# Performance work log

Measured on AMD Instinct MI355X. Metric: run time of the kernel, lower is better.

## Reference

```python
import jax, jax.numpy as jnp
import numpy as np

SR = 16000
N_FFT = 512
HOP = 160
WIN = 320
N_MELS = 80
FMIN = 0.0
FMAX = 8000.0
PAD_TO = 8
BLANK = 27.0
PREEMPH = 0.97
LOG_EPS = 2.0 ** -24
STD_EPS = 1e-5


def _hz_to_mel(f):
    # Slaney mel scale (librosa default, htk=False)
    f = np.asarray(f, dtype=np.float64)
    f_sp = 200.0 / 3.0
    mels = f / f_sp
    min_log_hz = 1000.0
    min_log_mel = min_log_hz / f_sp
    logstep = np.log(6.4) / 27.0
    return np.where(f >= min_log_hz,
                    min_log_mel + np.log(np.maximum(f, 1e-10) / min_log_hz) / logstep,
                    mels)


def _mel_to_hz(m):
    m = np.asarray(m, dtype=np.float64)
    f_sp = 200.0 / 3.0
    freqs = m * f_sp
    min_log_hz = 1000.0
    min_log_mel = min_log_hz / f_sp
    logstep = np.log(6.4) / 27.0
    return np.where(m >= min_log_mel,
                    min_log_hz * np.exp(logstep * (m - min_log_mel)),
                    freqs)


def mel_filterbank():
    # librosa.filters.mel(16000, 512, n_mels=80, fmin=0, fmax=8000), slaney norm
    fftfreqs = np.linspace(0.0, SR / 2.0, 1 + N_FFT // 2)
    mel_f = _mel_to_hz(np.linspace(_hz_to_mel(FMIN), _hz_to_mel(FMAX), N_MELS + 2))
    fdiff = np.diff(mel_f)
    ramps = mel_f[:, None] - fftfreqs[None, :]
    lower = -ramps[:-2] / fdiff[:-1, None]
    upper = ramps[2:] / fdiff[1:, None]
    weights = np.maximum(0.0, np.minimum(lower, upper))
    enorm = 2.0 / (mel_f[2:N_MELS + 2] - mel_f[:N_MELS])  # slaney norm
    weights *= enorm[:, None]
    return weights.astype(np.float32)  # [80, 257]


def _window():
    # periodic hann of length 320, zero-padded to 512 (centered), as in nnAudio STFT
    n = np.arange(WIN)
    w = 0.5 - 0.5 * np.cos(2.0 * np.pi * n / WIN)
    pad = (N_FFT - WIN) // 2
    return np.pad(w, (pad, pad)).astype(np.float32)  # [512]


def setup_inputs() -> dict:
    key = jax.random.key(0)
    k1, k2 = jax.random.split(key)
    B, L = 32, 240000
    x = 0.1 * jax.random.normal(k1, (B, L), dtype=jnp.float32)
    xn = jax.random.randint(k2, (B,), 160000, L + 1, dtype=jnp.int64)
    filterbank = jnp.asarray(mel_filterbank())
    return {"x": x, "xn": xn, "filterbank": filterbank}


def reference(x, xn, filterbank):
    B, L = x.shape
    seq_len = (xn // HOP + 1).astype(jnp.int64)  # floor((L+pad-512)/160)+1, pad=512

    # pre-emphasis (eval mode: dither=0)
    y = jnp.concatenate([x[:, :1], x[:, 1:] - PREEMPH * x[:, :-1]], axis=1)

    # center=True reflect pad by n_fft//2
    y = jnp.pad(y, ((0, 0), (N_FFT // 2, N_FFT // 2)), mode="reflect")

    # frame: T = L//HOP + 1
    T = L // HOP + 1
    idx = jnp.arange(T)[:, None] * HOP + jnp.arange(N_FFT)[None, :]  # [T, 512]
    frames = y[:, idx]  # [B, T, 512]
    win = jnp.asarray(_window())
    spec = jnp.fft.rfft(frames * win, axis=-1)  # [B, T, 257] complex
    power = jnp.real(spec) ** 2 + jnp.imag(spec) ** 2  # |X|^2 (sqrt then ^2 in torch)

    mel = jnp.einsum("mf,btf->bmt", filterbank, power)  # [B, 80, T]
    logmel = jnp.log(mel + LOG_EPS)

    # ragged per-sample, per-feature mean/std (std unbiased, ddof=1) over valid frames
    valid = (jnp.arange(T)[None, :] < seq_len[:, None]).astype(logmel.dtype)  # [B, T]
    n = seq_len.astype(logmel.dtype)[:, None]  # [B, 1]
    vm = valid[:, None, :]  # [B, 1, T]
    mean = jnp.sum(logmel * vm, axis=-1) / n  # [B, 80]
    centered = (logmel - mean[..., None]) * vm
    var = jnp.sum(centered * centered, axis=-1) / (n - 1.0)
    std = jnp.sqrt(var) + STD_EPS
    out = (logmel - mean[..., None]) / std[..., None]

    # zero out invalid frames, then pad T to multiple of PAD_TO with BLANK
    out = out * vm
    pad_amt = T % PAD_TO
    if pad_amt != 0:
        out = jnp.pad(out, ((0, 0), (0, 0), (0, PAD_TO - pad_amt)),
                      constant_values=BLANK)
    return out, seq_len
```

## Files before the change

### kernel.cpp

```cpp
#include <hip/hip_runtime.h>
#include <math.h>

constexpr int BATCH = 32;
constexpr int LEN   = 240000;
constexpr int HOPS  = 160;
constexpr int T     = 1501;
constexpr int TOUT  = 1504;
constexpr int NMEL  = 80;
constexpr int NBIN  = 257;
constexpr int PAIRS = 751;
constexpr int CMAX  = 20;
constexpr int WSTR  = 25;
constexpr int P1OFF = 520;
constexpr float PRE     = 0.97f;
constexpr float LOG_EPS = 5.9604644775390625e-08f;
constexpr float STD_EPS = 1e-5f;
constexpr float BLANK_V = 27.0f;

constexpr size_t LOGMEL_ELTS = (size_t)BATCH * T * NMEL;

struct cpx { float r, i; };
__device__ __forceinline__ cpx cmul(cpx a, cpx b){ return {a.r*b.r - a.i*b.i, a.r*b.i + a.i*b.r}; }
__device__ __forceinline__ cpx cadd(cpx a, cpx b){ return {a.r+b.r, a.i+b.i}; }
__device__ __forceinline__ cpx csub(cpx a, cpx b){ return {a.r-b.r, a.i-b.i}; }

__device__ __forceinline__ void dft8(cpx* a) {
  const float s = 0.70710678118654752f;
  cpx b0 = cadd(a[0],a[4]), b1 = cadd(a[1],a[5]), b2 = cadd(a[2],a[6]), b3 = cadd(a[3],a[7]);
  cpx t0 = csub(a[0],a[4]), t1 = csub(a[1],a[5]), t2 = csub(a[2],a[6]), t3 = csub(a[3],a[7]);
  cpx e0 = t0;
  cpx e1 = { s*(t1.r + t1.i), s*(t1.i - t1.r) };
  cpx e2 = { t2.i, -t2.r };
  cpx e3 = { s*(t3.i - t3.r), -s*(t3.r + t3.i) };
  cpx c0 = cadd(b0,b2), c1 = cadd(b1,b3), c2 = csub(b0,b2), c3 = csub(b1,b3);
  cpx f0 = cadd(e0,e2), f1 = cadd(e1,e3), f2 = csub(e0,e2), f3 = csub(e1,e3);
  a[0] = cadd(c0,c1); a[4] = csub(c0,c1);
  a[2] = { c2.r + c3.i, c2.i - c3.r }; a[6] = { c2.r - c3.i, c2.i + c3.r };
  a[1] = cadd(f0,f1); a[5] = csub(f0,f1);
  a[3] = { f2.r + f3.i, f2.i - f3.r }; a[7] = { f2.r - f3.i, f2.i + f3.r };
}

__device__ __forceinline__ int read_n(const int* xn32, int b) {
  int probe = xn32[1];
  int v = (probe == 0) ? xn32[2 * b] : xn32[b];
  return v / HOPS + 1;
}

__global__ __launch_bounds__(64) void k_prep(const float* __restrict__ fb,
                                             int* __restrict__ lc,
                                             float* __restrict__ wg,
                                             float* __restrict__ ps) {
  const int m = blockIdx.x;
  const int l = threadIdx.x;
  ps[m * 64 + l] = 0.f;
  int first = 1 << 20, last = -1;
  for (int it = 0; it < 5; ++it) {
    int f = it * 64 + l;
    float w = (f < NBIN) ? fb[m * NBIN + f] : 0.f;
    unsigned long long mk = __ballot(w != 0.f);
    if (mk) {
      int lo = __ffsll(mk) - 1;
      int hi = 63 - __clzll(mk);
      if (first > NBIN) first = it * 64 + lo;
      last = it * 64 + hi;
    }
  }
  int cnt = (last >= first) ? last - first + 1 : 0;
  if (cnt > CMAX) cnt = CMAX;
  if (first > NBIN) first = 0;
  if (l == 0) lc[m] = first | (cnt << 16);
  if (l < CMAX) wg[m * CMAX + l] = (l < cnt) ? fb[m * NBIN + first + l] : 0.f;
}

__global__ __launch_bounds__(256) void k_logmel(const float* __restrict__ x,
    const int* __restrict__ lc, const float* __restrict__ wg,
    const int* __restrict__ xn32,
    float* __restrict__ logmel, float* __restrict__ ps) {
  __shared__ float shw[512];
  __shared__ float swg[NMEL * WSTR];
  __shared__ int   slc[NMEL];
  __shared__ float W[4][1024];
  __shared__ float vbuf[4][160];
  __shared__ int   sbw[4];

  const int tid = threadIdx.x;
  const int wid = tid >> 6;
  const int l   = tid & 63;

  for (int i = tid; i < 512; i += 256) {
    float w = 0.f;
    if (i >= 96 && i < 416)
      w = 0.5f - 0.5f * __cosf((float)(i - 96) * (6.283185307179586f / 320.f));
    shw[i] = w;
  }
  for (int i = tid; i < NMEL * CMAX; i += 256)
    swg[(i / CMAX) * WSTR + (i % CMAX)] = wg[i];
  if (tid < NMEL) slc[tid] = lc[tid];
  __syncthreads();

  float* Tre = W[wid];
  float* Tim = Tre + 512;

  const int pair = blockIdx.x * 4 + wid;
  const int b  = pair / PAIRS;
  const int q  = pair % PAIRS;
  const int t0 = 2 * q;
  const float* xb = x + (size_t)b * LEN;
  const int nb = read_n(xn32, b);

  cpx a[8];
  const int s0x = t0 * HOPS - 161;
  const bool interior = (s0x >= 0) && (s0x + 480 < LEN);
  if (interior) {
    for (int i = l; i < 481; i += 64) Tre[i] = xb[s0x + i];
    __builtin_amdgcn_wave_barrier();
    #pragma unroll
    for (int j = 0; j < 8; ++j) {
      int n = l + 64 * j;
      cpx z = {0.f, 0.f};
      if (n >= 96 && n < 416) {
        float w = shw[n];
        z.r = w * (Tre[n - 95] - PRE * Tre[n - 96]);
        z.i = w * (Tre[n + 65] - PRE * Tre[n + 64]);
      }
      a[j] = z;
    }
    __builtin_amdgcn_wave_barrier();
  } else {
    #pragma unroll
    for (int j = 0; j < 8; ++j) {
      int n = l + 64 * j;
      cpx z = {0.f, 0.f};
      if (n >= 96 && n < 416) {
        float w = shw[n];
        int p0 = t0 * HOPS + n - 256;
        int p1 = p0 + HOPS;
        int q0 = p0 < 0 ? -p0 : (p0 >= LEN ? 2 * LEN - 2 - p0 : p0);
        int q1 = p1 < 0 ? -p1 : (p1 >= LEN ? 2 * LEN - 2 - p1 : p1);
        float y0 = (q0 == 0) ? xb[0] : (xb[q0] - PRE * xb[q0 - 1]);
        float y1 = (q1 == 0) ? xb[0] : (xb[q1] - PRE * xb[q1 - 1]);
        z.r = w * y0; z.i = w * y1;
      }
      a[j] = z;
    }
  }

  dft8(a);
  {
    float sv, cv; __sincosf(-6.283185307179586f * (float)l / 512.f, &sv, &cv);
    cpx w1 = {cv, sv}, cur = w1;
    #pragma unroll
    for (int p = 1; p < 8; ++p) { a[p] = cmul(a[p], cur); cur = cmul(cur, w1); }
  }
  #pragma unroll
  for (int p = 0; p < 8; ++p) { int idx = 64 * p + (l ^ (8 * p)); Tre[idx] = a[p].r; Tim[idx] = a[p].i; }
  __builtin_amdgcn_wave_barrier();

  const int ph = l >> 3, lo8 = l & 7;
  #pragma unroll
  for (int m2 = 0; m2 < 8; ++m2) {
    int idx = 64 * ph + ((lo8 + 8 * m2) ^ (8 * ph));
    a[m2] = {Tre[idx], Tim[idx]};
  }
  dft8(a);
  {
    float sv, cv; __sincosf(-6.283185307179586f * (float)lo8 / 64.f, &sv, &cv);
    cpx w1 = {cv, sv}, cur = w1;
    #pragma unroll
    for (int r = 1; r < 8; ++r) { a[r] = cmul(a[r], cur); cur = cmul(cur, w1); }
  }
  __builtin_amdgcn_wave_barrier();
  #pragma unroll
  for (int r = 0; r < 8; ++r) { int idx = 64 * ph + 8 * (r ^ ph) + (lo8 ^ ph); Tre[idx] = a[r].r; Tim[idx] = a[r].i; }
  __builtin_amdgcn_wave_barrier();
  #pragma unroll
  for (int m1 = 0; m1 < 8; ++m1) {
    int idx = 64 * ph + 8 * (lo8 ^ ph) + (m1 ^ ph);
    a[m1] = {Tre[idx], Tim[idx]};
  }
  dft8(a);
  __builtin_amdgcn_wave_barrier();
  #pragma unroll
  for (int s = 0; s < 8; ++s) { int k = ph + 8 * lo8 + 64 * s; Tre[k] = a[s].r; Tim[k] = a[s].i; }
  __builtin_amdgcn_wave_barrier();

  float P0[4], P1[4];
  #pragma unroll
  for (int c = 0; c < 4; ++c) {
    int k  = l + 64 * c;
    int km = (512 - k) & 511;
    float zr = Tre[k], zi = Tim[k], mr = Tre[km], mi = Tim[km];
    float f0r = 0.5f * (zr + mr), f0i = 0.5f * (zi - mi);
    float f1r = 0.5f * (zi + mi), f1i = 0.5f * (mr - zr);
    P0[c] = f0r * f0r + f0i * f0i;
    P1[c] = f1r * f1r + f1i * f1i;
  }
  float pN0 = 0.f, pN1 = 0.f;
  if (l == 0) { float zr = Tre[256], zi = Tim[256]; pN0 = zr * zr; pN1 = zi * zi; }
  __builtin_amdgcn_wave_barrier();
  #pragma unroll
  for (int c = 0; c < 4; ++c) { int k = l + 64 * c; Tre[k] = P0[c]; Tre[P1OFF + k] = P1[c]; }
  if (l == 0) { Tre[256] = pN0; Tre[P1OFF + 256] = pN1; }
  __builtin_amdgcn_wave_barrier();

  auto melrow = [&](int f, int m) -> float {
    int meta = slc[m];
    int lo = meta & 0xffff;
    const float* pw = &swg[m * WSTR];
    const float* pp = &Tre[(f ? P1OFF : 0) + lo];
    float acc = 0.f;
    #pragma unroll
    for (int j = 0; j < CMAX; ++j) acc += pp[j] * pw[j];
    return __logf(acc + LOG_EPS);
  };

  size_t base0 = ((size_t)b * T + t0) * NMEL;
  {
    float lv = melrow(0, l);
    logmel[base0 + l] = lv;
    vbuf[wid][l] = (t0 < nb) ? lv : 0.f;
  }
  {
    bool ok = (t0 + 1) < T;
    float lv = ok ? melrow(1, l) : 0.f;
    if (ok) logmel[base0 + NMEL + l] = lv;
    vbuf[wid][80 + l] = (ok && (t0 + 1) < nb) ? lv : 0.f;
  }
  if (l < 32) {
    int f = l >> 4, m = 64 + (l & 15);
    bool ok = (t0 + f) < T;
    float lv = ok ? melrow(f, m) : 0.f;
    if (ok) logmel[base0 + (size_t)f * NMEL + m] = lv;
    vbuf[wid][f * 80 + m] = (ok && (t0 + f) < nb) ? lv : 0.f;
  }
  if (l == 0) sbw[wid] = b;
  __syncthreads();

  if (tid < NMEL) {
    const int b0 = (blockIdx.x * 4) / PAIRS;
    const bool strad = ((blockIdx.x * 4 + 3) / PAIRS) != b0;
    float s0 = 0.f, q0 = 0.f, s1 = 0.f, q1 = 0.f;
    #pragma unroll
    for (int w = 0; w < 4; ++w) {
      float v0 = vbuf[w][tid], v1 = vbuf[w][80 + tid];
      if (sbw[w] == b0) { s0 += v0 + v1; q0 += v0 * v0 + v1 * v1; }
      else              { s1 += v0 + v1; q1 += v0 * v0 + v1 * v1; }
    }
    atomicAdd(&ps[b0 * 160 + tid], s0);
    atomicAdd(&ps[b0 * 160 + 80 + tid], q0);
    if (strad) {
      atomicAdd(&ps[(b0 + 1) * 160 + tid], s1);
      atomicAdd(&ps[(b0 + 1) * 160 + 80 + tid], q1);
    }
  }
}

__global__ __launch_bounds__(256) void k_apply(const float* __restrict__ logmel,
    const float* __restrict__ ps, const int* __restrict__ xn32,
    float* __restrict__ out, float* __restrict__ outseq) {
  const int bid = blockIdx.x;
  const int b = bid / 47, c = bid % 47;
  const int tbase = c * 32;
  __shared__ float tile[32 * 81];
  __shared__ float smean[80], sistd[80];
  const int tid = threadIdx.x;
  const int n = read_n(xn32, b);
  if (tid < 80) {
    float S = ps[b * 160 + tid], S2 = ps[b * 160 + 80 + tid];
    float fn = (float)n;
    float mean = S / fn;
    float var = (S2 - fn * mean * mean) / (fn - 1.f);
    var = var < 0.f ? 0.f : var;
    smean[tid] = mean;
    sistd[tid] = 1.f / (sqrtf(var) + STD_EPS);
  }
  __syncthreads();

  for (int e = tid; e < 640; e += 256) {
    int tt = e / 20, v = e % 20;
    int t = tbase + tt;
    int m0 = 4 * v;
    float4 val;
    if (t >= T)      val = make_float4(BLANK_V, BLANK_V, BLANK_V, BLANK_V);
    else if (t >= n) val = make_float4(0.f, 0.f, 0.f, 0.f);
    else {
      const float4 g = *(const float4*)&logmel[((size_t)b * T + t) * NMEL + m0];
      val.x = (g.x - smean[m0])     * sistd[m0];
      val.y = (g.y - smean[m0 + 1]) * sistd[m0 + 1];
      val.z = (g.z - smean[m0 + 2]) * sistd[m0 + 2];
      val.w = (g.w - smean[m0 + 3]) * sistd[m0 + 3];
    }
    float* tp = &tile[tt * 81 + m0];
    tp[0] = val.x; tp[1] = val.y; tp[2] = val.z; tp[3] = val.w;
  }
  __syncthreads();
  for (int e = tid; e < 640; e += 256) {
    int m = e >> 3, v = e & 7;
    int tt0 = 4 * v;
    float4 o;
    o.x = tile[(tt0    ) * 81 + m];
    o.y = tile[(tt0 + 1) * 81 + m];
    o.z = tile[(tt0 + 2) * 81 + m];
    o.w = tile[(tt0 + 3) * 81 + m];
    *(float4*)&out[((size_t)b * NMEL + m) * TOUT + tbase + tt0] = o;
  }
  if (c == 0 && tid == 0) outseq[b] = (float)n;
}

extern "C" void kernel_launch(void* const* d_in, const int* in_sizes, int n_in,
                              void* d_out, int out_size, void* d_ws, size_t ws_size,
                              hipStream_t stream) {
  const float* x  = (const float*)d_in[0];
  const int*   xn = (const int*)d_in[1];
  const float* fb = (const float*)d_in[2];

  float* out    = (float*)d_out;
  float* outseq = out + (size_t)BATCH * NMEL * TOUT;

  float* logmel = (float*)d_ws;
  int*   lc = (int*)(logmel + LOGMEL_ELTS);
  float* wg = (float*)(lc + NMEL);
  float* ps = wg + NMEL * CMAX;

  k_prep  <<<NMEL, 64, 0, stream>>>(fb, lc, wg, ps);
  k_logmel<<<(BATCH * PAIRS) / 4, 256, 0, stream>>>(x, lc, wg, xn, logmel, ps);
  k_apply <<<BATCH * 47, 256, 0, stream>>>(logmel, ps, xn, out, outseq);
}
```

Before: 131.3 us.

## Interleave complex data as float2 in LDS and pack mel pair compute

Stores FFT scratch as interleaved float2 (real, imag) instead of split real and imag planes, so each LDS access moves a complex pair. The power spectra of the two frames are packed into float2 so one mel dot-product loop serves both frames. The Hann window is now computed inline rather than held in a shared table, and the k_logmel launch bounds request 6 blocks per SM. k_apply tiles 64 frames per block instead of 32, which halves the block count and needs a bounds guard on the tail tile.

```diff
diff --git a/kernel.cpp b/kernel.cpp
--- a/kernel.cpp
+++ b/kernel.cpp
@@ -10,8 +10,7 @@
 constexpr int NBIN  = 257;
 constexpr int PAIRS = 751;
 constexpr int CMAX  = 20;
-constexpr int WSTR  = 25;
-constexpr int P1OFF = 520;
+constexpr int WSTR  = 21;
 constexpr float PRE     = 0.97f;
 constexpr float LOG_EPS = 5.9604644775390625e-08f;
 constexpr float STD_EPS = 1e-5f;
@@ -19,25 +18,35 @@
 
 constexpr size_t LOGMEL_ELTS = (size_t)BATCH * T * NMEL;
 
-struct cpx { float r, i; };
-__device__ __forceinline__ cpx cmul(cpx a, cpx b){ return {a.r*b.r - a.i*b.i, a.r*b.i + a.i*b.r}; }
-__device__ __forceinline__ cpx cadd(cpx a, cpx b){ return {a.r+b.r, a.i+b.i}; }
-__device__ __forceinline__ cpx csub(cpx a, cpx b){ return {a.r-b.r, a.i-b.i}; }
-
-__device__ __forceinline__ void dft8(cpx* a) {
+typedef __attribute__((ext_vector_type(2))) float v2f;
+
+__device__ __forceinline__ v2f cmul(v2f a, v2f b) {
+  v2f r;
+  r.x = a.x * b.x - a.y * b.y;
+  r.y = a.x * b.y + a.y * b.x;
+  return r;
+}
+
+__device__ __forceinline__ void dft8(v2f* a) {
   const float s = 0.70710678118654752f;
-  cpx b0 = cadd(a[0],a[4]), b1 = cadd(a[1],a[5]), b2 = cadd(a[2],a[6]), b3 = cadd(a[3],a[7]);
-  cpx t0 = csub(a[0],a[4]), t1 = csub(a[1],a[5]), t2 = csub(a[2],a[6]), t3 = csub(a[3],a[7]);
-  cpx e0 = t0;
-  cpx e1 = { s*(t1.r + t1.i), s*(t1.i - t1.r) };
-  cpx e2 = { t2.i, -t2.r };
-  cpx e3 = { s*(t3.i - t3.r), -s*(t3.r + t3.i) };
-  cpx c0 = cadd(b0,b2), c1 = cadd(b1,b3), c2 = csub(b0,b2), c3 = csub(b1,b3);
-  cpx f0 = cadd(e0,e2), f1 = cadd(e1,e3), f2 = csub(e0,e2), f3 = csub(e1,e3);
-  a[0] = cadd(c0,c1); a[4] = csub(c0,c1);
-  a[2] = { c2.r + c3.i, c2.i - c3.r }; a[6] = { c2.r - c3.i, c2.i + c3.r };
-  a[1] = cadd(f0,f1); a[5] = csub(f0,f1);
-  a[3] = { f2.r + f3.i, f2.i - f3.r }; a[7] = { f2.r - f3.i, f2.i + f3.r };
+  v2f b0 = a[0] + a[4], b1 = a[1] + a[5], b2 = a[2] + a[6], b3 = a[3] + a[7];
+  v2f t0 = a[0] - a[4], t1 = a[1] - a[5], t2 = a[2] - a[6], t3 = a[3] - a[7];
+  v2f e0 = t0, e1, e2, e3;
+  e1.x = s * (t1.x + t1.y); e1.y = s * (t1.y - t1.x);
+  e2.x = t2.y;              e2.y = -t2.x;
+  e3.x = s * (t3.y - t3.x); e3.y = -s * (t3.x + t3.y);
+  v2f c0 = b0 + b2, c1 = b1 + b3, c2 = b0 - b2, c3 = b1 - b3;
+  v2f f0 = e0 + e2, f1 = e1 + e3, f2 = e0 - e2, f3 = e1 - e3;
+  a[0] = c0 + c1; a[4] = c0 - c1;
+  a[2].x = c2.x + c3.y; a[2].y = c2.y - c3.x;
+  a[6].x = c2.x - c3.y; a[6].y = c2.y + c3.x;
+  a[1] = f0 + f1; a[5] = f0 - f1;
+  a[3].x = f2.x + f3.y; a[3].y = f2.y - f3.x;
+  a[7].x = f2.x - f3.y; a[7].y = f2.y + f3.x;
+}
+
+__device__ __forceinline__ float hann(int n) {
+  return 0.5f - 0.5f * __cosf((float)(n - 96) * (6.283185307179586f / 320.f));
 }
 
 __device__ __forceinline__ int read_n(const int* xn32, int b) {
@@ -72,34 +81,26 @@
   if (l < CMAX) wg[m * CMAX + l] = (l < cnt) ? fb[m * NBIN + first + l] : 0.f;
 }
 
-__global__ __launch_bounds__(256) void k_logmel(const float* __restrict__ x,
+__global__ __launch_bounds__(256, 6) void k_logmel(const float* __restrict__ x,
     const int* __restrict__ lc, const float* __restrict__ wg,
     const int* __restrict__ xn32,
     float* __restrict__ logmel, float* __restrict__ ps) {
-  __shared__ float shw[512];
+  __shared__ v2f   Wv[4][512];
   __shared__ float swg[NMEL * WSTR];
   __shared__ int   slc[NMEL];
-  __shared__ float W[4][1024];
-  __shared__ float vbuf[4][160];
+  __shared__ v2f   vbuf[4][NMEL];
   __shared__ int   sbw[4];
 
   const int tid = threadIdx.x;
   const int wid = tid >> 6;
   const int l   = tid & 63;
 
-  for (int i = tid; i < 512; i += 256) {
-    float w = 0.f;
-    if (i >= 96 && i < 416)
-      w = 0.5f - 0.5f * __cosf((float)(i - 96) * (6.283185307179586f / 320.f));
-    shw[i] = w;
-  }
   for (int i = tid; i < NMEL * CMAX; i += 256)
     swg[(i / CMAX) * WSTR + (i % CMAX)] = wg[i];
   if (tid < NMEL) slc[tid] = lc[tid];
   __syncthreads();
 
-  float* Tre = W[wid];
-  float* Tim = Tre + 512;
+  v2f* Wvw = Wv[wid];
 
   const int pair = blockIdx.x * 4 + wid;
   const int b  = pair / PAIRS;
@@ -108,20 +109,23 @@
   const float* xb = x + (size_t)b * LEN;
   const int nb = read_n(xn32, b);
 
-  cpx a[8];
+  v2f a[8];
   const int s0x = t0 * HOPS - 161;
   const bool interior = (s0x >= 0) && (s0x + 480 < LEN);
   if (interior) {
-    for (int i = l; i < 481; i += 64) Tre[i] = xb[s0x + i];
+    float* Ts = (float*)Wvw;
+    for (int i = l; i < 481; i += 64) Ts[i] = xb[s0x + i];
     __builtin_amdgcn_wave_barrier();
     #pragma unroll
     for (int j = 0; j < 8; ++j) {
       int n = l + 64 * j;
-      cpx z = {0.f, 0.f};
+      v2f z = {0.f, 0.f};
       if (n >= 96 && n < 416) {
-        float w = shw[n];
-        z.r = w * (Tre[n - 95] - PRE * Tre[n - 96]);
-        z.i = w * (Tre[n + 65] - PRE * Tre[n + 64]);
+        float w = hann(n);
+        v2f y;
+        y.x = Ts[n - 95] - PRE * Ts[n - 96];
+        y.y = Ts[n + 65] - PRE * Ts[n + 64];
+        z = y * w;
       }
       a[j] = z;
     }
@@ -130,16 +134,17 @@
     #pragma unroll
     for (int j = 0; j < 8; ++j) {
       int n = l + 64 * j;
-      cpx z = {0.f, 0.f};
+      v2f z = {0.f, 0.f};
       if (n >= 96 && n < 416) {
-        float w = shw[n];
+        float w = hann(n);
         int p0 = t0 * HOPS + n - 256;
         int p1 = p0 + HOPS;
         int q0 = p0 < 0 ? -p0 : (p0 >= LEN ? 2 * LEN - 2 - p0 : p0);
         int q1 = p1 < 0 ? -p1 : (p1 >= LEN ? 2 * LEN - 2 - p1 : p1);
-        float y0 = (q0 == 0) ? xb[0] : (xb[q0] - PRE * xb[q0 - 1]);
-        float y1 = (q1 == 0) ? xb[0] : (xb[q1] - PRE * xb[q1 - 1]);
-        z.r = w * y0; z.i = w * y1;
+        v2f y;
+        y.x = (q0 == 0) ? xb[0] : (xb[q0] - PRE * xb[q0 - 1]);
+        y.y = (q1 == 0) ? xb[0] : (xb[q1] - PRE * xb[q1 - 1]);
+        z = y * w;
       }
       a[j] = z;
     }
@@ -148,90 +153,87 @@
   dft8(a);
   {
     float sv, cv; __sincosf(-6.283185307179586f * (float)l / 512.f, &sv, &cv);
-    cpx w1 = {cv, sv}, cur = w1;
+    v2f w1 = {cv, sv}, cur = w1;
     #pragma unroll
     for (int p = 1; p < 8; ++p) { a[p] = cmul(a[p], cur); cur = cmul(cur, w1); }
   }
   #pragma unroll
-  for (int p = 0; p < 8; ++p) { int idx = 64 * p + (l ^ (8 * p)); Tre[idx] = a[p].r; Tim[idx] = a[p].i; }
+  for (int p = 0; p < 8; ++p) Wvw[64 * p + (l ^ (8 * p))] = a[p];
   __builtin_amdgcn_wave_barrier();
 
   const int ph = l >> 3, lo8 = l & 7;
   #pragma unroll
-  for (int m2 = 0; m2 < 8; ++m2) {
-    int idx = 64 * ph + ((lo8 + 8 * m2) ^ (8 * ph));
-    a[m2] = {Tre[idx], Tim[idx]};
-  }
+  for (int m2 = 0; m2 < 8; ++m2)
+    a[m2] = Wvw[64 * ph + ((lo8 + 8 * m2) ^ (8 * ph))];
   dft8(a);
   {
     float sv, cv; __sincosf(-6.283185307179586f * (float)lo8 / 64.f, &sv, &cv);
-    cpx w1 = {cv, sv}, cur = w1;
+    v2f w1 = {cv, sv}, cur = w1;
     #pragma unroll
     for (int r = 1; r < 8; ++r) { a[r] = cmul(a[r], cur); cur = cmul(cur, w1); }
   }
   __builtin_amdgcn_wave_barrier();
   #pragma unroll
-  for (int r = 0; r < 8; ++r) { int idx = 64 * ph + 8 * (r ^ ph) + (lo8 ^ ph); Tre[idx] = a[r].r; Tim[idx] = a[r].i; }
-  __builtin_amdgcn_wave_barrier();
-  #pragma unroll
-  for (int m1 = 0; m1 < 8; ++m1) {
-    int idx = 64 * ph + 8 * (lo8 ^ ph) + (m1 ^ ph);
-    a[m1] = {Tre[idx], Tim[idx]};
-  }
+  for (int r = 0; r < 8; ++r) Wvw[64 * ph + 8 * (r ^ ph) + (lo8 ^ ph)] = a[r];
+  __builtin_amdgcn_wave_barrier();
+  #pragma unroll
+  for (int m1 = 0; m1 < 8; ++m1)
+    a[m1] = Wvw[64 * ph + 8 * (lo8 ^ ph) + (m1 ^ ph)];
   dft8(a);
   __builtin_amdgcn_wave_barrier();
   #pragma unroll
-  for (int s = 0; s < 8; ++s) { int k = ph + 8 * lo8 + 64 * s; Tre[k] = a[s].r; Tim[k] = a[s].i; }
-  __builtin_amdgcn_wave_barrier();
-
-  float P0[4], P1[4];
+  for (int s = 0; s < 8; ++s) Wvw[ph + 8 * lo8 + 64 * s] = a[s];
+  __builtin_amdgcn_wave_barrier();
+
+  v2f Ppk[4];
   #pragma unroll
   for (int c = 0; c < 4; ++c) {
     int k  = l + 64 * c;
     int km = (512 - k) & 511;
-    float zr = Tre[k], zi = Tim[k], mr = Tre[km], mi = Tim[km];
-    float f0r = 0.5f * (zr + mr), f0i = 0.5f * (zi - mi);
-    float f1r = 0.5f * (zi + mi), f1i = 0.5f * (mr - zr);
-    P0[c] = f0r * f0r + f0i * f0i;
-    P1[c] = f1r * f1r + f1i * f1i;
-  }
-  float pN0 = 0.f, pN1 = 0.f;
-  if (l == 0) { float zr = Tre[256], zi = Tim[256]; pN0 = zr * zr; pN1 = zi * zi; }
-  __builtin_amdgcn_wave_barrier();
-  #pragma unroll
-  for (int c = 0; c < 4; ++c) { int k = l + 64 * c; Tre[k] = P0[c]; Tre[P1OFF + k] = P1[c]; }
-  if (l == 0) { Tre[256] = pN0; Tre[P1OFF + 256] = pN1; }
-  __builtin_amdgcn_wave_barrier();
-
-  auto melrow = [&](int f, int m) -> float {
-    int meta = slc[m];
-    int lo = meta & 0xffff;
+    v2f z = Wvw[k], mz = Wvw[km];
+    float f0r = 0.5f * (z.x + mz.x), f0i = 0.5f * (z.y - mz.y);
+    float f1r = 0.5f * (z.y + mz.y), f1i = 0.5f * (mz.x - z.x);
+    Ppk[c].x = f0r * f0r + f0i * f0i;
+    Ppk[c].y = f1r * f1r + f1i * f1i;
+  }
+  v2f pN = {0.f, 0.f};
+  if (l == 0) { v2f zN = Wvw[256]; pN.x = zN.x * zN.x; pN.y = zN.y * zN.y; }
+  __builtin_amdgcn_wave_barrier();
+  #pragma unroll
+  for (int c = 0; c < 4; ++c) Wvw[l + 64 * c] = Ppk[c];
+  if (l == 0) Wvw[256] = pN;
+  __builtin_amdgcn_wave_barrier();
+
+  auto melpk = [&](int m) -> v2f {
+    int lo = slc[m] & 0xffff;
     const float* pw = &swg[m * WSTR];
-    const float* pp = &Tre[(f ? P1OFF : 0) + lo];
-    float acc = 0.f;
+    const v2f* pp = &Wvw[lo];
+    v2f acc = {0.f, 0.f};
     #pragma unroll
     for (int j = 0; j < CMAX; ++j) acc += pp[j] * pw[j];
-    return __logf(acc + LOG_EPS);
+    return acc;
   };
 
+  const bool ok1 = (t0 + 1) < T;
   size_t base0 = ((size_t)b * T + t0) * NMEL;
   {
-    float lv = melrow(0, l);
-    logmel[base0 + l] = lv;
-    vbuf[wid][l] = (t0 < nb) ? lv : 0.f;
-  }
-  {
-    bool ok = (t0 + 1) < T;
-    float lv = ok ? melrow(1, l) : 0.f;
-    if (ok) logmel[base0 + NMEL + l] = lv;
-    vbuf[wid][80 + l] = (ok && (t0 + 1) < nb) ? lv : 0.f;
-  }
-  if (l < 32) {
-    int f = l >> 4, m = 64 + (l & 15);
-    bool ok = (t0 + f) < T;
-    float lv = ok ? melrow(f, m) : 0.f;
-    if (ok) logmel[base0 + (size_t)f * NMEL + m] = lv;
-    vbuf[wid][f * 80 + m] = (ok && (t0 + f) < nb) ? lv : 0.f;
+    v2f acc = melpk(l);
+    float lv0 = __logf(acc.x + LOG_EPS);
+    float lv1 = __logf(acc.y + LOG_EPS);
+    logmel[base0 + l] = lv0;
+    if (ok1) logmel[base0 + NMEL + l] = lv1;
+    v2f v; v.x = (t0 < nb) ? lv0 : 0.f; v.y = (t0 + 1 < nb) ? lv1 : 0.f;
+    vbuf[wid][l] = v;
+  }
+  if (l < 16) {
+    int m = 64 + l;
+    v2f acc = melpk(m);
+    float lv0 = __logf(acc.x + LOG_EPS);
+    float lv1 = __logf(acc.y + LOG_EPS);
+    logmel[base0 + m] = lv0;
+    if (ok1) logmel[base0 + NMEL + m] = lv1;
+    v2f v; v.x = (t0 < nb) ? lv0 : 0.f; v.y = (t0 + 1 < nb) ? lv1 : 0.f;
+    vbuf[wid][m] = v;
   }
   if (l == 0) sbw[wid] = b;
   __syncthreads();
@@ -242,9 +244,9 @@
     float s0 = 0.f, q0 = 0.f, s1 = 0.f, q1 = 0.f;
     #pragma unroll
     for (int w = 0; w < 4; ++w) {
-      float v0 = vbuf[w][tid], v1 = vbuf[w][80 + tid];
-      if (sbw[w] == b0) { s0 += v0 + v1; q0 += v0 * v0 + v1 * v1; }
-      else              { s1 += v0 + v1; q1 += v0 * v0 + v1 * v1; }
+      v2f v = vbuf[w][tid];
+      if (sbw[w] == b0) { s0 += v.x + v.y; q0 += v.x * v.x + v.y * v.y; }
+      else              { s1 += v.x + v.y; q1 += v.x * v.x + v.y * v.y; }
     }
     atomicAdd(&ps[b0 * 160 + tid], s0);
     atomicAdd(&ps[b0 * 160 + 80 + tid], q0);
@@ -259,9 +261,9 @@
     const float* __restrict__ ps, const int* __restrict__ xn32,
     float* __restrict__ out, float* __restrict__ outseq) {
   const int bid = blockIdx.x;
-  const int b = bid / 47, c = bid % 47;
-  const int tbase = c * 32;
-  __shared__ float tile[32 * 81];
+  const int b = bid / 24, c = bid % 24;
+  const int tbase = c * 64;
+  __shared__ float tile[64 * 81];
   __shared__ float smean[80], sistd[80];
   const int tid = threadIdx.x;
   const int n = read_n(xn32, b);
@@ -276,7 +278,7 @@
   }
   __syncthreads();
 
-  for (int e = tid; e < 640; e += 256) {
+  for (int e = tid; e < 1280; e += 256) {
     int tt = e / 20, v = e % 20;
     int t = tbase + tt;
     int m0 = 4 * v;
@@ -294,15 +296,18 @@
     tp[0] = val.x; tp[1] = val.y; tp[2] = val.z; tp[3] = val.w;
   }
   __syncthreads();
-  for (int e = tid; e < 640; e += 256) {
-    int m = e >> 3, v = e & 7;
+  for (int e = tid; e < 1280; e += 256) {
+    int m = e >> 4, v = e & 15;
     int tt0 = 4 * v;
-    float4 o;
-    o.x = tile[(tt0    ) * 81 + m];
-    o.y = tile[(tt0 + 1) * 81 + m];
-    o.z = tile[(tt0 + 2) * 81 + m];
-    o.w = tile[(tt0 + 3) * 81 + m];
-    *(float4*)&out[((size_t)b * NMEL + m) * TOUT + tbase + tt0] = o;
+    int t = tbase + tt0;
+    if (t < TOUT) {
+      float4 o;
+      o.x = tile[(tt0    ) * 81 + m];
+      o.y = tile[(tt0 + 1) * 81 + m];
+      o.z = tile[(tt0 + 2) * 81 + m];
+      o.w = tile[(tt0 + 3) * 81 + m];
+      *(float4*)&out[((size_t)b * NMEL + m) * TOUT + t] = o;
+    }
   }
   if (c == 0 && tid == 0) outseq[b] = (float)n;
 }
@@ -324,5 +329,5 @@
 
   k_prep  <<<NMEL, 64, 0, stream>>>(fb, lc, wg, ps);
   k_logmel<<<(BATCH * PAIRS) / 4, 256, 0, stream>>>(x, lc, wg, xn, logmel, ps);
-  k_apply <<<BATCH * 47, 256, 0, stream>>>(logmel, ps, xn, out, outseq);
-}
+  k_apply <<<BATCH * 24, 256, 0, stream>>>(logmel, ps, xn, out, outseq);
+}
```

Result: faster. 128.3 us (-2.3%).
